# Kernel optimization log

Measured on AMD Instinct MI355X. Metric: run time of the kernel, lower is better.

Reference implementation:

```python
import jax, jax.numpy as jnp
import numpy as np

EPS = 1e-5
NHEAD = 8

def layernorm(x, g, b):
    m = x.mean(-1, keepdims=True)
    v = ((x - m) ** 2).mean(-1, keepdims=True)
    return (x - m) * jax.lax.rsqrt(v + EPS) * g + b


def setup_inputs() -> dict:
    key = jax.random.key(0)
    ks = jax.random.split(key, 20)
    D, F, K, G, NC, FF, B = 768, 2048, 100, 10, 1000, 2048, 128
    s = lambda k, shape, scale: jax.random.normal(k, shape, jnp.float32) * scale
    return {
        "x": s(ks[0], (B, F, 7, 7), 1.0),
        "W_embed": s(ks[1], (F, D), 0.02), "b_embed": jnp.zeros((D,), jnp.float32),
        "query_embed": s(ks[2], (K, D), 1.0),
        "wq": s(ks[3], (D, D), 0.03), "wk": s(ks[4], (D, D), 0.03), "wv": s(ks[5], (D, D), 0.03),
        "bq": jnp.zeros((D,), jnp.float32), "bk": jnp.zeros((D,), jnp.float32), "bv": jnp.zeros((D,), jnp.float32),
        "wo": s(ks[6], (D, D), 0.03), "bo": jnp.zeros((D,), jnp.float32),
        "w1": s(ks[7], (D, FF), 0.03), "b1": jnp.zeros((FF,), jnp.float32),
        "w2": s(ks[8], (FF, D), 0.02), "b2": jnp.zeros((D,), jnp.float32),
        "g1": jnp.ones((D,), jnp.float32), "be1": jnp.zeros((D,), jnp.float32),
        "g2": jnp.ones((D,), jnp.float32), "be2": jnp.zeros((D,), jnp.float32),
        "g3": jnp.ones((D,), jnp.float32), "be3": jnp.zeros((D,), jnp.float32),
        "dup_pool": s(ks[9], (K, D, G), 0.03),
        "dup_bias": jnp.zeros((NC,), jnp.float32),
    }


def reference(x, W_embed, b_embed, query_embed, wq, wk, wv, bq, bk, bv, wo, bo,
              w1, b1, w2, b2, g1, be1, g2, be2, g3, be3, dup_pool, dup_bias):
    B = x.shape[0]
    D = W_embed.shape[1]
    H = NHEAD
    hd = D // H
    num_classes = dup_bias.shape[0]

    # [B, 2048, 7, 7] -> [B, 49, 2048] -> [B, 49, 768], relu
    mem = x.reshape(B, x.shape[1], -1).transpose(0, 2, 1)
    mem = jax.nn.relu(mem @ W_embed + b_embed)          # (B, S, D)

    # queries broadcast to batch (batch-first internally)
    tgt = jnp.broadcast_to(query_embed[None], (B,) + query_embed.shape)  # (B, K, D)

    # tgt = tgt + dropout1(tgt) -> 2*tgt in eval; then norm1
    tgt = layernorm(2.0 * tgt, g1, be1)

    # cross multi-head attention: Q=tgt, K=V=mem
    q = (tgt @ wq + bq).reshape(B, -1, H, hd)
    k = (mem @ wk + bk).reshape(B, -1, H, hd)
    v = (mem @ wv + bv).reshape(B, -1, H, hd)
    scores = jnp.einsum("bkhd,bshd->bhks", q, k) / jnp.sqrt(jnp.float32(hd))
    attn = jax.nn.softmax(scores, axis=-1)
    ctx = jnp.einsum("bhks,bshd->bkhd", attn, v).reshape(B, -1, D)
    attn_out = ctx @ wo + bo

    tgt = layernorm(tgt + attn_out, g2, be2)

    # FFN
    ff = jax.nn.relu(tgt @ w1 + b1) @ w2 + b2
    h = layernorm(tgt + ff, g3, be3)                    # (B, K, D)

    # GroupFC: per-group matmul, batched as one einsum
    out_extrap = jnp.einsum("bkd,kdg->bkg", h, dup_pool)  # (B, K, G)
    logits = out_extrap.reshape(B, -1)[:, :num_classes] + dup_bias
    return logits
```

## Files before the change

kernel.cpp:

```cpp
#include <hip/hip_runtime.h>
#include <math.h>

#define D_MODEL 768
#define HEADS   8
#define HDIM    96
#define SEQ     49
#define KQ      100
#define NB      128
#define FDIM    2048
#define FFD     2048
#define GRP     10
#define NCLS    1000

typedef unsigned short ushort_t;
typedef unsigned int uint_t;
typedef __attribute__((ext_vector_type(8))) short short8;
typedef __attribute__((ext_vector_type(4))) float f32x4;

__device__ __forceinline__ float bf2f(ushort_t u) {
    uint_t x = ((uint_t)u) << 16;
    return __uint_as_float(x);
}
__device__ __forceinline__ ushort_t f2bf(float f) {
    uint_t x = __float_as_uint(f);
    x += 0x7fffu + ((x >> 16) & 1u);
    return (ushort_t)(x >> 16);
}

__device__ __forceinline__ void gld_lds16(const void* g, void* l) {
    __builtin_amdgcn_global_load_lds(
        (const __attribute__((address_space(1))) unsigned int*)g,
        (__attribute__((address_space(3))) unsigned int*)l, 16, 0, 0);
}

template <int MT>
__global__ __launch_bounds__(256, 4) void gemm_bf16(
    const ushort_t* __restrict__ A, const ushort_t* __restrict__ Bt,
    const float* __restrict__ bias, const float* __restrict__ bias2,
    ushort_t* __restrict__ C, ushort_t* __restrict__ C2,
    int M, int N, int K, int nsplit, int relu, float scale,
    const ushort_t* __restrict__ resid, int rmode)
{
    constexpr int BM  = MT * 32;
    constexpr int ACH = MT * 4;
    constexpr int NCH = (ACH + 16) / 4;

    __shared__ ushort_t As[BM * 64];
    __shared__ ushort_t Bs[128 * 64];

    const int tid  = threadIdx.x;
    const int w    = tid >> 6;
    const int lane = tid & 63;
    const int quad = lane >> 4;
    const int l16  = lane & 15;

    const int nx = gridDim.x, NY = gridDim.y;
    const int bid = blockIdx.y * nx + blockIdx.x;
    const int NYmain = NY & ~7;
    const int Tmain = NYmain * nx;
    int r, c;
    if (bid < Tmain) {
        const int grp = bid / (8 * nx);
        const int rem = bid - grp * 8 * nx;
        r = grp * 8 + (rem & 7);
        c = rem >> 3;
    } else {
        const int rem = bid - Tmain;
        r = NYmain + rem / nx;
        c = rem - (rem / nx) * nx;
    }
    const int rowBase = r * BM;
    const int nBase   = c * 128;
    const int wr = (w >> 1) * (MT * 16);
    const int wc = (w & 1) * 64;

    const float* biasb;
    ushort_t* Cb;
    int coff, ldcb;
    if (nBase < nsplit) { biasb = bias;  Cb = C;  coff = 0;      ldcb = nsplit; }
    else                { biasb = bias2; Cb = C2; coff = nsplit; ldcb = N - nsplit; }

    f32x4 acc[MT][4];
#pragma unroll
    for (int i = 0; i < MT; i++)
#pragma unroll
        for (int j = 0; j < 4; j++) acc[i][j] = (f32x4){0.f, 0.f, 0.f, 0.f};

    const int lrow = lane >> 3;
    const int ksub = ((lane & 7) ^ ((lane >> 3) & 7)) * 8;

    const ushort_t* gp[NCH];
    ushort_t* lp[NCH];
#pragma unroll
    for (int i = 0; i < NCH; i++) {
        int ch = w + 4 * i;
        if (ch < ACH) {
            int rr = min(rowBase + ch * 8 + lrow, M - 1);
            gp[i] = A + (size_t)rr * K + ksub;
            lp[i] = As + ch * 512 + lane * 8;
        } else {
            int cb = ch - ACH;
            int rr = nBase + cb * 8 + lrow;
            gp[i] = Bt + (size_t)rr * K + ksub;
            lp[i] = Bs + cb * 512 + lane * 8;
        }
    }

    const int swl = l16 & 7;

    for (int k0 = 0; k0 < K; k0 += 64) {
#pragma unroll
        for (int i = 0; i < NCH; i++) gld_lds16(gp[i] + k0, lp[i]);
        __syncthreads();

#pragma unroll
        for (int s = 0; s < 2; s++) {
            const int ks = ((4 * s + quad) ^ swl) * 8;
            short8 af[MT], bfr[4];
#pragma unroll
            for (int mt = 0; mt < MT; mt++)
                af[mt] = *(const short8*)(As + (wr + mt * 16 + l16) * 64 + ks);
#pragma unroll
            for (int nt = 0; nt < 4; nt++)
                bfr[nt] = *(const short8*)(Bs + (wc + nt * 16 + l16) * 64 + ks);
#pragma unroll
            for (int mt = 0; mt < MT; mt++)
#pragma unroll
                for (int nt = 0; nt < 4; nt++)
                    acc[mt][nt] = __builtin_amdgcn_mfma_f32_16x16x32_bf16(
                        af[mt], bfr[nt], acc[mt][nt], 0, 0, 0);
        }
        __syncthreads();
    }

#pragma unroll
    for (int nt = 0; nt < 4; nt++) {
        const int colg = nBase + wc + nt * 16 + l16;
        const int col  = colg - coff;
        const float bv = biasb[col];
#pragma unroll
        for (int mt = 0; mt < MT; mt++) {
#pragma unroll
            for (int rg = 0; rg < 4; rg++) {
                const int row = rowBase + wr + mt * 16 + quad * 4 + rg;
                if (row < M) {
                    float v = (acc[mt][nt][rg] + bv) * scale;
                    if (relu) v = fmaxf(v, 0.f);
                    if (rmode) {
                        int rrow = (rmode == 2) ? (row % KQ) : row;
                        v += bf2f(resid[(size_t)rrow * D_MODEL + col]);
                    }
                    Cb[(size_t)row * ldcb + col] = f2bf(v);
                }
            }
        }
    }
}

__global__ __launch_bounds__(256) void prep_all(
    const float* __restrict__ We, const float* __restrict__ wq,
    const float* __restrict__ wk, const float* __restrict__ wv,
    const float* __restrict__ wo, const float* __restrict__ w1,
    const float* __restrict__ w2, const float* __restrict__ x,
    ushort_t* __restrict__ Wet, ushort_t* __restrict__ wqt,
    ushort_t* __restrict__ wkt, ushort_t* __restrict__ wvt,
    ushort_t* __restrict__ wot, ushort_t* __restrict__ w1t,
    ushort_t* __restrict__ w2t, ushort_t* __restrict__ xb)
{
    __shared__ __align__(16) char smem[25600];
    int t = blockIdx.x;
    if (t < 1728) {
        float* tile = (float*)smem;
        const float* src; ushort_t* dst; int K, N, tx;
        if (t < 384)       {           src = We; dst = Wet; K = 2048; N = 768;  tx = 12; }
        else if (t < 528)  { t -= 384; src = wq; dst = wqt; K = 768;  N = 768;  tx = 12; }
        else if (t < 672)  { t -= 528; src = wk; dst = wkt; K = 768;  N = 768;  tx = 12; }
        else if (t < 816)  { t -= 672; src = wv; dst = wvt; K = 768;  N = 768;  tx = 12; }
        else if (t < 960)  { t -= 816; src = wo; dst = wot; K = 768;  N = 768;  tx = 12; }
        else if (t < 1344) { t -= 960; src = w1; dst = w1t; K = 768;  N = 2048; tx = 32; }
        else               { t -= 1344; src = w2; dst = w2t; K = 2048; N = 768; tx = 12; }
        const int n0 = (t % tx) * 64, k0 = (t / tx) * 64;
        const int tr = threadIdx.x >> 6, tc = threadIdx.x & 63;
#pragma unroll
        for (int i = 0; i < 16; i++) {
            int r = i * 4 + tr;
            tile[r * 65 + tc] = src[(size_t)(k0 + r) * N + n0 + tc];
        }
        __syncthreads();
#pragma unroll
        for (int i = 0; i < 16; i++) {
            int nr = i * 4 + tr;
            dst[(size_t)(n0 + nr) * K + k0 + tc] = f2bf(tile[tc * 65 + nr]);
        }
    } else {
        ushort_t* tile = (ushort_t*)smem;
        int bx = t - 1728;
        const int b = bx >> 3, f0 = (bx & 7) * 256, tt = threadIdx.x;
        const float* src = x + ((size_t)b * FDIM + f0 + tt) * SEQ;
#pragma unroll
        for (int s = 0; s < SEQ; s++) tile[tt * 50 + s] = f2bf(src[s]);
        __syncthreads();
        for (int s = 0; s < SEQ; s++)
            xb[(size_t)(b * SEQ + s) * FDIM + f0 + tt] = tile[tt * 50 + s];
    }
}

__global__ __launch_bounds__(256) void ln4(
    const void* __restrict__ in, int in_bf16,
    const float* __restrict__ g, const float* __restrict__ be,
    ushort_t* __restrict__ out, float pre_scale, int nrows)
{
    const int w = threadIdx.x >> 6, lane = threadIdx.x & 63;
    const int row = blockIdx.x * 4 + w;
    if (row >= nrows) return;

    float v[12];
    if (in_bf16) {
        const uint_t* p = (const uint_t*)in + (size_t)row * 384;
#pragma unroll
        for (int i = 0; i < 6; i++) {
            uint_t u = p[lane + i * 64];
            v[2 * i]     = bf2f((ushort_t)(u & 0xffff)) * pre_scale;
            v[2 * i + 1] = bf2f((ushort_t)(u >> 16)) * pre_scale;
        }
    } else {
        const float2* p = (const float2*)((const float*)in + (size_t)row * D_MODEL);
#pragma unroll
        for (int i = 0; i < 6; i++) {
            float2 t = p[lane + i * 64];
            v[2 * i] = t.x * pre_scale;
            v[2 * i + 1] = t.y * pre_scale;
        }
    }
    float s = 0.f;
#pragma unroll
    for (int i = 0; i < 12; i++) s += v[i];
#pragma unroll
    for (int off = 32; off > 0; off >>= 1) s += __shfl_xor(s, off);
    const float mean = s * (1.f / D_MODEL);
    float q = 0.f;
#pragma unroll
    for (int i = 0; i < 12; i++) { float d = v[i] - mean; q += d * d; }
#pragma unroll
    for (int off = 32; off > 0; off >>= 1) q += __shfl_xor(q, off);
    const float rstd = rsqrtf(q * (1.f / D_MODEL) + 1e-5f);

    const float2* g2 = (const float2*)g;
    const float2* b2 = (const float2*)be;
    uint_t* op = (uint_t*)out + (size_t)row * 384;
#pragma unroll
    for (int i = 0; i < 6; i++) {
        int j = lane + i * 64;
        float2 gg = g2[j], bb = b2[j];
        ushort_t lo = f2bf((v[2 * i] - mean) * rstd * gg.x + bb.x);
        ushort_t hi = f2bf((v[2 * i + 1] - mean) * rstd * gg.y + bb.y);
        op[j] = (uint_t)lo | ((uint_t)hi << 16);
    }
}

__global__ __launch_bounds__(256) void attn_mfma(
    const ushort_t* __restrict__ q, const ushort_t* __restrict__ k,
    const ushort_t* __restrict__ v, ushort_t* __restrict__ ctx)
{
    __shared__ ushort_t Pt[128][72];
    __shared__ ushort_t Vt[96][72];

    const int bh = blockIdx.x;
    const int b = bh >> 3, h = bh & 7;
    const int tid = threadIdx.x;
    const int w = tid >> 6, lane = tid & 63;
    const int quad = lane >> 4, l16 = lane & 15;
    const int mrow0 = 32 * w;

    for (int idx = tid; idx < 96 * 64; idx += 256) {
        int d = idx >> 6, s = idx & 63;
        ushort_t val = 0;
        if (s < SEQ) val = v[(size_t)(b * SEQ + s) * D_MODEL + h * HDIM + d];
        Vt[d][s] = val;
    }

    f32x4 accS[2][4];
#pragma unroll
    for (int i = 0; i < 2; i++)
#pragma unroll
        for (int j = 0; j < 4; j++) accS[i][j] = (f32x4){0.f, 0.f, 0.f, 0.f};

#pragma unroll
    for (int k0 = 0; k0 < HDIM; k0 += 32) {
        short8 af[2], bfr[4];
#pragma unroll
        for (int mt = 0; mt < 2; mt++) {
            int kq = min(mrow0 + mt * 16 + l16, KQ - 1);
            af[mt] = *(const short8*)(q + (size_t)kq * D_MODEL + h * HDIM + k0 + quad * 8);
        }
#pragma unroll
        for (int nt = 0; nt < 4; nt++) {
            int s = min(nt * 16 + l16, SEQ - 1);
            bfr[nt] = *(const short8*)(k + (size_t)(b * SEQ + s) * D_MODEL + h * HDIM + k0 + quad * 8);
        }
#pragma unroll
        for (int mt = 0; mt < 2; mt++)
#pragma unroll
            for (int nt = 0; nt < 4; nt++)
                accS[mt][nt] = __builtin_amdgcn_mfma_f32_16x16x32_bf16(
                    af[mt], bfr[nt], accS[mt][nt], 0, 0, 0);
    }

#pragma unroll
    for (int mt = 0; mt < 2; mt++) {
#pragma unroll
        for (int r = 0; r < 4; r++) {
            float vals[4];
            float vmax = -1e30f;
#pragma unroll
            for (int nt = 0; nt < 4; nt++) {
                vals[nt] = accS[mt][nt][r];
                if (nt * 16 + l16 < SEQ) vmax = fmaxf(vmax, vals[nt]);
            }
#pragma unroll
            for (int off = 1; off < 16; off <<= 1)
                vmax = fmaxf(vmax, __shfl_xor(vmax, off));
            float p[4], psum = 0.f;
#pragma unroll
            for (int nt = 0; nt < 4; nt++) {
                float e = (nt * 16 + l16 < SEQ) ? __expf(vals[nt] - vmax) : 0.f;
                p[nt] = e;
                psum += e;
            }
#pragma unroll
            for (int off = 1; off < 16; off <<= 1)
                psum += __shfl_xor(psum, off);
            const float inv = 1.f / psum;
            const int row = mrow0 + mt * 16 + quad * 4 + r;
#pragma unroll
            for (int nt = 0; nt < 4; nt++)
                Pt[row][nt * 16 + l16] = f2bf(p[nt] * inv);
        }
    }
    __syncthreads();

    f32x4 accO[2][6];
#pragma unroll
    for (int i = 0; i < 2; i++)
#pragma unroll
        for (int j = 0; j < 6; j++) accO[i][j] = (f32x4){0.f, 0.f, 0.f, 0.f};

#pragma unroll
    for (int k0 = 0; k0 < 64; k0 += 32) {
        short8 af[2], bfr[6];
#pragma unroll
        for (int mt = 0; mt < 2; mt++)
            af[mt] = *(const short8*)(&Pt[mrow0 + mt * 16 + l16][k0 + quad * 8]);
#pragma unroll
        for (int nt = 0; nt < 6; nt++)
            bfr[nt] = *(const short8*)(&Vt[nt * 16 + l16][k0 + quad * 8]);
#pragma unroll
        for (int mt = 0; mt < 2; mt++)
#pragma unroll
            for (int nt = 0; nt < 6; nt++)
                accO[mt][nt] = __builtin_amdgcn_mfma_f32_16x16x32_bf16(
                    af[mt], bfr[nt], accO[mt][nt], 0, 0, 0);
    }

#pragma unroll
    for (int mt = 0; mt < 2; mt++) {
#pragma unroll
        for (int r = 0; r < 4; r++) {
            const int kq = mrow0 + mt * 16 + quad * 4 + r;
            if (kq < KQ) {
                size_t oa = (size_t)(b * KQ + kq) * D_MODEL + h * HDIM;
#pragma unroll
                for (int nt = 0; nt < 6; nt++)
                    ctx[oa + nt * 16 + l16] = f2bf(accO[mt][nt][r]);
            }
        }
    }
}

__global__ __launch_bounds__(256) void groupfc3(
    const ushort_t* __restrict__ hb, const float* __restrict__ dp,
    const float* __restrict__ dbias, const float* __restrict__ g3,
    const float* __restrict__ be3, float* __restrict__ out)
{
    __shared__ float dps[D_MODEL * 11];
    __shared__ float hsr[8][D_MODEL];
    __shared__ float gbs[2][D_MODEL];

    const int b0 = blockIdx.x * 8;
    const int kq = blockIdx.y;
    const int tid = threadIdx.x;

    for (int i = tid; i < D_MODEL * GRP; i += 256) {
        int d = i / GRP, g = i - d * GRP;
        dps[d * 11 + g] = dp[(size_t)kq * (D_MODEL * GRP) + i];
    }
    for (int i = tid; i < D_MODEL; i += 256) {
        gbs[0][i] = g3[i];
        gbs[1][i] = be3[i];
    }
#pragma unroll
    for (int bb = 0; bb < 8; bb++) {
#pragma unroll
        for (int i = 0; i < 3; i++) {
            int d = tid + i * 256;
            hsr[bb][d] = bf2f(hb[(size_t)((b0 + bb) * KQ + kq) * D_MODEL + d]);
        }
    }
    __syncthreads();

    const int w = tid >> 6, lane = tid & 63;

#pragma unroll
    for (int rr = 0; rr < 2; rr++) {
        const int r = w * 2 + rr;
        float v[12];
        float s = 0.f;
#pragma unroll
        for (int i = 0; i < 12; i++) { v[i] = hsr[r][lane + i * 64]; s += v[i]; }
#pragma unroll
        for (int off = 32; off > 0; off >>= 1) s += __shfl_xor(s, off);
        const float mean = s * (1.f / D_MODEL);
        float q = 0.f;
#pragma unroll
        for (int i = 0; i < 12; i++) { float d = v[i] - mean; q += d * d; }
#pragma unroll
        for (int off = 32; off > 0; off >>= 1) q += __shfl_xor(q, off);
        const float rstd = rsqrtf(q * (1.f / D_MODEL) + 1e-5f);
#pragma unroll
        for (int i = 0; i < 12; i++) {
            int d = lane + i * 64;
            hsr[r][d] = (v[i] - mean) * rstd * gbs[0][d] + gbs[1][d];
        }
    }
    __syncthreads();

    for (int item = w; item < 8 * GRP; item += 4) {
        int bb = item / GRP, g = item - bb * GRP;
        float a = 0.f;
#pragma unroll
        for (int i = 0; i < 12; i++) {
            int d = lane + i * 64;
            a = fmaf(hsr[bb][d], dps[d * 11 + g], a);
        }
#pragma unroll
        for (int off = 32; off > 0; off >>= 1) a += __shfl_down(a, off);
        if (lane == 0)
            out[(size_t)(b0 + bb) * NCLS + kq * GRP + g] = a + dbias[kq * GRP + g];
    }
}

extern "C" void kernel_launch(void* const* d_in, const int* in_sizes, int n_in,
                              void* d_out, int out_size, void* d_ws, size_t ws_size,
                              hipStream_t stream)
{
    const float* x   = (const float*)d_in[0];
    const float* We  = (const float*)d_in[1];
    const float* be_ = (const float*)d_in[2];
    const float* qe  = (const float*)d_in[3];
    const float* wq  = (const float*)d_in[4];
    const float* wk  = (const float*)d_in[5];
    const float* wv  = (const float*)d_in[6];
    const float* bq  = (const float*)d_in[7];
    const float* bk  = (const float*)d_in[8];
    const float* bv  = (const float*)d_in[9];
    const float* wo  = (const float*)d_in[10];
    const float* bo  = (const float*)d_in[11];
    const float* w1  = (const float*)d_in[12];
    const float* b1  = (const float*)d_in[13];
    const float* w2  = (const float*)d_in[14];
    const float* b2  = (const float*)d_in[15];
    const float* g1  = (const float*)d_in[16];
    const float* be1 = (const float*)d_in[17];
    const float* g2  = (const float*)d_in[18];
    const float* be2 = (const float*)d_in[19];
    const float* g3  = (const float*)d_in[20];
    const float* be3 = (const float*)d_in[21];
    const float* dp  = (const float*)d_in[22];
    const float* db  = (const float*)d_in[23];
    float* out = (float*)d_out;
    ushort_t* ws = (ushort_t*)d_ws;

    ushort_t* xb  = ws;
    ushort_t* mem = xb + 12845056;
    ushort_t* kb  = mem + 4816896;
    ushort_t* vb  = kb + 4816896;
    ushort_t* ffh = ws;
    ushort_t* rB  = ws + 27295744;
    ushort_t* Wet = rB;
    ushort_t* wqt = Wet + 1572864;
    ushort_t* wkt = wqt + 589824;
    ushort_t* wvt = wkt + 589824;
    ushort_t* wot = wvt + 589824;
    ushort_t* w1t = wot + 589824;
    ushort_t* w2t = w1t + 1572864;
    ushort_t* tgt = w2t + 1572864;
    ushort_t* qb  = tgt + 76800;
    ushort_t* ctx = qb + 76800;
    ushort_t* t2  = ctx + 9830400;
    ushort_t* hb  = t2 + 9830400;

    dim3 blk(256);
    const float qscale = 1.0f / sqrtf((float)HDIM);

    prep_all<<<dim3(2752), blk, 0, stream>>>(We, wq, wk, wv, wo, w1, w2, x,
                                             Wet, wqt, wkt, wvt, wot, w1t, w2t, xb);

    gemm_bf16<2><<<dim3(6, 98), blk, 0, stream>>>(xb, Wet, be_, be_, mem, mem,
                                                  6272, 768, 2048, 768, 1, 1.f, nullptr, 0);
    ln4<<<dim3(25), blk, 0, stream>>>(qe, 0, g1, be1, tgt, 2.0f, KQ);
    gemm_bf16<1><<<dim3(6, 4), blk, 0, stream>>>(tgt, wqt, bq, bq, qb, qb,
                                                 KQ, 768, 768, 768, 0, qscale, nullptr, 0);
    gemm_bf16<2><<<dim3(12, 98), blk, 0, stream>>>(mem, wkt, bk, bv, kb, vb,
                                                   6272, 1536, 768, 768, 0, 1.f, nullptr, 0);
    attn_mfma<<<dim3(NB * HEADS), blk, 0, stream>>>(qb, kb, vb, ctx);
    gemm_bf16<2><<<dim3(6, 200), blk, 0, stream>>>(ctx, wot, bo, bo, t2, t2,
                                                   12800, 768, 768, 768, 0, 1.f, tgt, 2);
    ln4<<<dim3(3200), blk, 0, stream>>>(t2, 1, g2, be2, t2, 1.0f, 12800);
    gemm_bf16<2><<<dim3(16, 200), blk, 0, stream>>>(t2, w1t, b1, b1, ffh, ffh,
                                                    12800, 2048, 768, 2048, 1, 1.f, nullptr, 0);
    gemm_bf16<2><<<dim3(6, 200), blk, 0, stream>>>(ffh, w2t, b2, b2, hb, hb,
                                                   12800, 768, 2048, 768, 0, 1.f, t2, 1);
    groupfc3<<<dim3(16, KQ), blk, 0, stream>>>(hb, dp, db, g3, be3, out);
}
```

Baseline: 503.8 us.

## Add 256x256-tile 512-thread GEMM with phased MFMA/prefetch interleave for big GEMMs

```diff
diff --git a/kernel.cpp b/kernel.cpp
--- a/kernel.cpp
+++ b/kernel.cpp
@@ -145,6 +145,203 @@
                 const int row = rowBase + wr + mt * 16 + quad * 4 + rg;
                 if (row < M) {
                     float v = (acc[mt][nt][rg] + bv) * scale;
+                    if (relu) v = fmaxf(v, 0.f);
+                    if (rmode) {
+                        int rrow = (rmode == 2) ? (row % KQ) : row;
+                        v += bf2f(resid[(size_t)rrow * D_MODEL + col]);
+                    }
+                    Cb[(size_t)row * ldcb + col] = f2bf(v);
+                }
+            }
+        }
+    }
+}
+
+__global__ __launch_bounds__(512, 2) void gemm256(
+    const ushort_t* __restrict__ A, const ushort_t* __restrict__ Bt,
+    const float* __restrict__ bias, const float* __restrict__ bias2,
+    ushort_t* __restrict__ C, ushort_t* __restrict__ C2,
+    int M, int N, int K, int nsplit, int relu, float scale,
+    const ushort_t* __restrict__ resid, int rmode)
+{
+    __shared__ ushort_t As[2][256 * 64];
+    __shared__ ushort_t Bs[2][256 * 64];
+
+    const int tid  = threadIdx.x;
+    const int w    = tid >> 6;
+    const int lane = tid & 63;
+    const int quad = lane >> 4;
+    const int l16  = lane & 15;
+
+    const int nx = gridDim.x, NY = gridDim.y;
+    const int bid = blockIdx.y * nx + blockIdx.x;
+    const int NYmain = NY & ~7;
+    const int Tmain = NYmain * nx;
+    int r, c;
+    if (bid < Tmain) {
+        const int grp = bid / (8 * nx);
+        const int rem = bid - grp * 8 * nx;
+        r = grp * 8 + (rem & 7);
+        c = rem >> 3;
+    } else {
+        const int rem = bid - Tmain;
+        r = NYmain + rem / nx;
+        c = rem - (rem / nx) * nx;
+    }
+    const int rowBase = r * 256;
+    const int nBase   = c * 256;
+    const int wr = (w >> 2) * 128;
+    const int wc = (w & 3) * 64;
+
+    const int srow = tid >> 3;
+    const int sch  = (tid & 7) ^ (srow & 7);
+    const ushort_t* gA[4];
+    const ushort_t* gB[4];
+#pragma unroll
+    for (int q = 0; q < 4; q++) {
+        const int lr = q * 64 + srow;
+        gA[q] = A  + (size_t)min(rowBase + lr, M - 1) * K + sch * 8;
+        gB[q] = Bt + (size_t)(nBase + lr) * K + sch * 8;
+    }
+    const int sdst = tid * 8;
+
+#define STA(u, q) gld_lds16(gA[q] + (size_t)(u) * 64, &As[(u) & 1][(q) * 4096 + sdst])
+#define STB(u, q) gld_lds16(gB[q] + (size_t)(u) * 64, &Bs[(u) & 1][(q) * 4096 + sdst])
+
+#define PH_BEGIN() do { __builtin_amdgcn_s_barrier();                       \
+        asm volatile("s_waitcnt lgkmcnt(0)" ::: "memory");                  \
+        __builtin_amdgcn_sched_barrier(0);                                  \
+        __builtin_amdgcn_s_setprio(1); } while (0)
+#define PH_END() do { __builtin_amdgcn_sched_barrier(0);                    \
+        __builtin_amdgcn_s_setprio(0);                                      \
+        __builtin_amdgcn_s_barrier(); } while (0)
+
+    f32x4 acc[8][4];
+#pragma unroll
+    for (int i = 0; i < 8; i++)
+#pragma unroll
+        for (int j = 0; j < 4; j++) acc[i][j] = (f32x4){0.f, 0.f, 0.f, 0.f};
+
+    const int swl = l16 & 7;
+    const int NT  = K >> 6;
+
+#pragma unroll
+    for (int q = 0; q < 4; q++) { STA(0, q); STB(0, q); }
+#pragma unroll
+    for (int q = 0; q < 4; q++) { STA(1, q); STB(1, q); }
+    asm volatile("s_waitcnt vmcnt(8)" ::: "memory");
+    __builtin_amdgcn_s_barrier();
+
+    for (int t = 0; t < NT; ++t) {
+        const int p = t & 1;
+        const ushort_t* Ap = As[p];
+        const ushort_t* Bp = Bs[p];
+        const bool pf = (t + 2) < NT;
+
+        short8 af[4][2], bf[2][2], bg[2][2];
+
+#pragma unroll
+        for (int i = 0; i < 4; i++)
+#pragma unroll
+            for (int s = 0; s < 2; s++)
+                af[i][s] = *(const short8*)(Ap + (wr + i * 16 + l16) * 64 +
+                                            (((4 * s + quad) ^ swl) * 8));
+#pragma unroll
+        for (int j = 0; j < 2; j++)
+#pragma unroll
+            for (int s = 0; s < 2; s++)
+                bf[j][s] = *(const short8*)(Bp + (wc + j * 16 + l16) * 64 +
+                                            (((4 * s + quad) ^ swl) * 8));
+        PH_BEGIN();
+#pragma unroll
+        for (int i = 0; i < 4; i++)
+#pragma unroll
+            for (int j = 0; j < 2; j++)
+#pragma unroll
+                for (int s = 0; s < 2; s++)
+                    acc[i][j] = __builtin_amdgcn_mfma_f32_16x16x32_bf16(
+                        af[i][s], bf[j][s], acc[i][j], 0, 0, 0);
+        PH_END();
+
+#pragma unroll
+        for (int j = 0; j < 2; j++)
+#pragma unroll
+            for (int s = 0; s < 2; s++)
+                bg[j][s] = *(const short8*)(Bp + (wc + (j + 2) * 16 + l16) * 64 +
+                                            (((4 * s + quad) ^ swl) * 8));
+        if (pf) { STA(t + 2, 0); STA(t + 2, 2); }
+        PH_BEGIN();
+#pragma unroll
+        for (int i = 0; i < 4; i++)
+#pragma unroll
+            for (int j = 0; j < 2; j++)
+#pragma unroll
+                for (int s = 0; s < 2; s++)
+                    acc[i][j + 2] = __builtin_amdgcn_mfma_f32_16x16x32_bf16(
+                        af[i][s], bg[j][s], acc[i][j + 2], 0, 0, 0);
+        PH_END();
+
+#pragma unroll
+        for (int i = 0; i < 4; i++)
+#pragma unroll
+            for (int s = 0; s < 2; s++)
+                af[i][s] = *(const short8*)(Ap + (wr + 64 + i * 16 + l16) * 64 +
+                                            (((4 * s + quad) ^ swl) * 8));
+        if (pf) { STB(t + 2, 0); STB(t + 2, 1); STB(t + 2, 2); STB(t + 2, 3); }
+        PH_BEGIN();
+#pragma unroll
+        for (int i = 0; i < 4; i++)
+#pragma unroll
+            for (int j = 0; j < 2; j++)
+#pragma unroll
+                for (int s = 0; s < 2; s++)
+                    acc[i + 4][j + 2] = __builtin_amdgcn_mfma_f32_16x16x32_bf16(
+                        af[i][s], bg[j][s], acc[i + 4][j + 2], 0, 0, 0);
+        PH_END();
+
+        if (pf) { STA(t + 2, 1); STA(t + 2, 3); }
+        __builtin_amdgcn_s_barrier();
+        asm volatile("s_waitcnt lgkmcnt(0)" ::: "memory");
+        __builtin_amdgcn_sched_barrier(0);
+        __builtin_amdgcn_s_setprio(1);
+#pragma unroll
+        for (int i = 0; i < 4; i++)
+#pragma unroll
+            for (int j = 0; j < 2; j++)
+#pragma unroll
+                for (int s = 0; s < 2; s++)
+                    acc[i + 4][j] = __builtin_amdgcn_mfma_f32_16x16x32_bf16(
+                        af[i][s], bf[j][s], acc[i + 4][j], 0, 0, 0);
+        __builtin_amdgcn_sched_barrier(0);
+        __builtin_amdgcn_s_setprio(0);
+        if (pf) asm volatile("s_waitcnt vmcnt(8)" ::: "memory");
+        else    asm volatile("s_waitcnt vmcnt(0)" ::: "memory");
+        __builtin_amdgcn_s_barrier();
+    }
+
+#undef STA
+#undef STB
+#undef PH_BEGIN
+#undef PH_END
+
+    const float* biasb;
+    ushort_t* Cb;
+    int coff, ldcb;
+    if (nBase < nsplit) { biasb = bias;  Cb = C;  coff = 0;      ldcb = nsplit; }
+    else                { biasb = bias2; Cb = C2; coff = nsplit; ldcb = N - nsplit; }
+
+#pragma unroll
+    for (int j = 0; j < 4; j++) {
+        const int colg = nBase + wc + j * 16 + l16;
+        const int col  = colg - coff;
+        const float bv = biasb[col];
+#pragma unroll
+        for (int i = 0; i < 8; i++) {
+#pragma unroll
+            for (int rg = 0; rg < 4; rg++) {
+                const int row = rowBase + wr + i * 16 + quad * 4 + rg;
+                if (row < M) {
+                    float v = (acc[i][j][rg] + bv) * scale;
                     if (relu) v = fmaxf(v, 0.f);
                     if (rmode) {
                         int rrow = (rmode == 2) ? (row % KQ) : row;
@@ -500,6 +697,7 @@
     ushort_t* hb  = t2 + 9830400;
 
     dim3 blk(256);
+    dim3 blk512(512);
     const float qscale = 1.0f / sqrtf((float)HDIM);
 
     prep_all<<<dim3(2752), blk, 0, stream>>>(We, wq, wk, wv, wo, w1, w2, x,
@@ -510,15 +708,15 @@
     ln4<<<dim3(25), blk, 0, stream>>>(qe, 0, g1, be1, tgt, 2.0f, KQ);
     gemm_bf16<1><<<dim3(6, 4), blk, 0, stream>>>(tgt, wqt, bq, bq, qb, qb,
                                                  KQ, 768, 768, 768, 0, qscale, nullptr, 0);
-    gemm_bf16<2><<<dim3(12, 98), blk, 0, stream>>>(mem, wkt, bk, bv, kb, vb,
-                                                   6272, 1536, 768, 768, 0, 1.f, nullptr, 0);
+    gemm256<<<dim3(6, 25), blk512, 0, stream>>>(mem, wkt, bk, bv, kb, vb,
+                                                6272, 1536, 768, 768, 0, 1.f, nullptr, 0);
     attn_mfma<<<dim3(NB * HEADS), blk, 0, stream>>>(qb, kb, vb, ctx);
-    gemm_bf16<2><<<dim3(6, 200), blk, 0, stream>>>(ctx, wot, bo, bo, t2, t2,
-                                                   12800, 768, 768, 768, 0, 1.f, tgt, 2);
+    gemm256<<<dim3(3, 50), blk512, 0, stream>>>(ctx, wot, bo, bo, t2, t2,
+                                                12800, 768, 768, 768, 0, 1.f, tgt, 2);
     ln4<<<dim3(3200), blk, 0, stream>>>(t2, 1, g2, be2, t2, 1.0f, 12800);
-    gemm_bf16<2><<<dim3(16, 200), blk, 0, stream>>>(t2, w1t, b1, b1, ffh, ffh,
-                                                    12800, 2048, 768, 2048, 1, 1.f, nullptr, 0);
-    gemm_bf16<2><<<dim3(6, 200), blk, 0, stream>>>(ffh, w2t, b2, b2, hb, hb,
-                                                   12800, 768, 2048, 768, 0, 1.f, t2, 1);
+    gemm256<<<dim3(8, 50), blk512, 0, stream>>>(t2, w1t, b1, b1, ffh, ffh,
+                                                12800, 2048, 768, 2048, 1, 1.f, nullptr, 0);
+    gemm256<<<dim3(3, 50), blk512, 0, stream>>>(ffh, w2t, b2, b2, hb, hb,
+                                                12800, 768, 2048, 768, 0, 1.f, t2, 1);
     groupfc3<<<dim3(16, KQ), blk, 0, stream>>>(hb, dp, db, g3, be3, out);
 }
```

New measurement: 605.5 us. 20.2% more time.
